# Kernel tuning notes

Hardware: AMD Instinct MI355X
Metric: run time of the kernel (lower is better)

The kernel has to match this reference:

```python
import jax, jax.numpy as jnp
import numpy as np

B, L, DL, DM, K = 8192, 1, 1024, 1024, 8


def setup_inputs() -> dict:
    key = jax.random.key(0)
    ks = jax.random.split(key, 8)
    s = lambda k, shape, sc=1.0: jax.random.normal(k, shape, jnp.float32) * sc
    return {
        "l_hidden": s(ks[0], (B, L, DL)),
        "m_hidden": s(ks[1], (B, L, DM)),
        "G_l_m": s(ks[2], (DL, K, DM)),   # randn'd each fwd in torch; exposed as input
        "G_m_l": s(ks[3], (DM, K, DL)),
        "l_fc1_w": s(ks[4], (256, DL), 0.02),
        "l_fc1_b": jnp.zeros((256,), jnp.float32),
        "l_fc2_w": s(ks[5], (DL, 256), 0.02),
        "l_fc2_b": jnp.zeros((DL,), jnp.float32),
        "m_fc1_w": s(ks[6], (128, DM), 0.02),
        "m_fc1_b": jnp.zeros((128,), jnp.float32),
        "m_fc2_w": s(ks[7], (DM, 128), 0.02),
        "m_fc2_b": jnp.zeros((DM,), jnp.float32),
    }


def _cross(h_a, h_b, G, g_vec):
    """One direction of the cross-share unit.
    h_a: [B,L,Da], h_b: [B,L,Db], G: [Da,K,Db], g_vec: [B,L,Da]. L must be 1.
    Broadcasts G over batch instead of torch's .repeat (same math, no 256GB copy).
    """
    b, l, da = h_a.shape
    k = G.shape[1]
    # l_hidden @ reshape(G, [Da, K*Db]) -> reshape to [B, L*K, Db]
    s = jnp.einsum('bld,dke->blke', h_a, G).reshape(b, l * k, -1)      # [B,L*K,Db]
    # tanh( shared @ h_b^T ) -> [B, L*K, L]
    t = jnp.tanh(jnp.einsum('bke,bse->bks', s, h_b))                    # [B,L*K,L]
    # reshape [B,L,K,L] -> permute [B,L,L,K] -> [B,L*L,K]
    t = t.reshape(b, l, k, l).transpose(0, 1, 3, 2).reshape(b, l * l, k)
    g = jnp.tile(g_vec, (1, k, 1))                                      # [B,L*K,Da] (L=1 -> [B,K,Da])
    vec = jnp.matmul(t, g)                                              # [B,L*L,Da]
    attn = jax.nn.softmax(vec, axis=-1)
    out = h_a + attn * h_a
    return out, attn


def reference(l_hidden, m_hidden, G_l_m, G_m_l,
              l_fc1_w, l_fc1_b, l_fc2_w, l_fc2_b,
              m_fc1_w, m_fc1_b, m_fc2_w, m_fc2_b):
    # dropout(0.3) is identity in eval mode
    G_vec_l = (l_hidden @ l_fc1_w.T + l_fc1_b) @ l_fc2_w.T + l_fc2_b   # [B,L,DL]
    G_vec_m = (m_hidden @ m_fc1_w.T + m_fc1_b) @ m_fc2_w.T + m_fc2_b   # [B,L,DM]
    l_out, l_attn = _cross(l_hidden, m_hidden, G_l_m, G_vec_l)
    m_out, m_attn = _cross(m_hidden, l_hidden, G_m_l, G_vec_m)
    return l_out, m_out, l_attn, m_attn
```

## Files before the change

### kernel.cpp

```cpp
#include <hip/hip_runtime.h>


#define NB 8192
#define DD 1024

typedef __bf16 bf16x8 __attribute__((ext_vector_type(8)));
typedef float f32x4 __attribute__((ext_vector_type(4)));

__device__ __forceinline__ unsigned short f2bf(float f) {
  unsigned u = __float_as_uint(f);
  u += 0x7FFFu + ((u >> 16) & 1u);
  return (unsigned short)(u >> 16);
}
__device__ __forceinline__ float bf2f(unsigned short h) {
  return __uint_as_float(((unsigned)h) << 16);
}

__global__ __launch_bounds__(256) void split_cast_k(
    const float* __restrict__ in, unsigned short* __restrict__ hi,
    unsigned short* __restrict__ lo, int n4) {
  int i = blockIdx.x * 256 + threadIdx.x;
  if (i >= n4) return;
  float4 v = reinterpret_cast<const float4*>(in)[i];
  float vv[4] = {v.x, v.y, v.z, v.w};
  unsigned short hh[4], ll[4];
#pragma unroll
  for (int c = 0; c < 4; ++c) {
    hh[c] = f2bf(vv[c]);
    ll[c] = f2bf(vv[c] - bf2f(hh[c]));
  }
  reinterpret_cast<ushort4*>(hi)[i] = make_ushort4(hh[0], hh[1], hh[2], hh[3]);
  reinterpret_cast<ushort4*>(lo)[i] = make_ushort4(ll[0], ll[1], ll[2], ll[3]);
}

__global__ __launch_bounds__(256) void transpose_split_k(
    const float* __restrict__ G, unsigned short* __restrict__ bhi,
    unsigned short* __restrict__ blo) {
  __shared__ float t[32][33];
  int c0 = blockIdx.x * 32;
  int d0 = blockIdx.y * 32;
  int tx = threadIdx.x & 31;
  int tg = threadIdx.x >> 5;
#pragma unroll
  for (int s = 0; s < 4; ++s) {
    int dr = tg * 4 + s;
    t[dr][tx] = G[(size_t)(d0 + dr) * 8192 + c0 + tx];
  }
  __syncthreads();
#pragma unroll
  for (int s = 0; s < 4; ++s) {
    int cr = tg * 4 + s;
    float v = t[tx][cr];
    size_t o = (size_t)(c0 + cr) * 1024 + d0 + tx;
    unsigned short h = f2bf(v);
    bhi[o] = h;
    blo[o] = f2bf(v - bf2f(h));
  }
}

__global__ __launch_bounds__(256) void wct_k(
    const float* __restrict__ w1, const float* __restrict__ b1,
    const float* __restrict__ w2, const float* __restrict__ b2, int J,
    unsigned short* __restrict__ bhi, unsigned short* __restrict__ blo,
    float* __restrict__ bc) {
  __shared__ float w2row[256];
  int n = blockIdx.x;
  int tid = threadIdx.x;
  if (tid < J) w2row[tid] = w2[n * J + tid];
  __syncthreads();
#pragma unroll
  for (int s = 0; s < 4; ++s) {
    int i = tid + s * 256;
    float acc = 0.f;
    for (int j = 0; j < J; ++j) acc = fmaf(w2row[j], w1[j * 1024 + i], acc);
    size_t o = (size_t)(8192 + n) * 1024 + i;
    unsigned short h = f2bf(acc);
    bhi[o] = h;
    blo[o] = f2bf(acc - bf2f(h));
  }
  if (tid == 0) {
    float acc = 0.f;
    for (int j = 0; j < J; ++j) acc = fmaf(w2row[j], b1[j], acc);
    bc[n] = acc + b2[n];
  }
}

#define SBAR() do { asm volatile("" ::: "memory"); __builtin_amdgcn_s_barrier(); asm volatile("" ::: "memory"); } while (0)
#define WAITV0() asm volatile("s_waitcnt vmcnt(0)" ::: "memory")

#define GLOAD(SRC, DST)                                              \
  __builtin_amdgcn_global_load_lds(                                  \
      (const __attribute__((address_space(1))) void*)(SRC),          \
      (__attribute__((address_space(3))) void*)(lds + (DST)), 16, 0, 0)

__global__ __launch_bounds__(512, 1) void gemm_k(
    const unsigned short* __restrict__ Ahi_, const unsigned short* __restrict__ Alo_,
    const unsigned short* __restrict__ Bhi_, const unsigned short* __restrict__ Blo_,
    const float* __restrict__ hb, float* __restrict__ gvec, float* __restrict__ x) {
  __shared__ __align__(16) char lds[131072];
  const char* Ah = (const char*)Ahi_;
  const char* Al = (const char*)Alo_;
  const char* Bh = (const char*)Bhi_;
  const char* Bl = (const char*)Blo_;

  const int tid = threadIdx.x;
  const int lane = tid & 63;
  const int wid = tid >> 6;
  const int wm = wid >> 2, wn = wid & 3;

  const int bid = blockIdx.x;
  const int xcd = bid & 7;
  const int j = bid >> 3;
  const int by = xcd * 4 + (j & 3);
  const int bx = j >> 2;
  const int m0 = by * 256;
  const int n0 = bx * 256;
  const bool isg = (n0 >= 8192);
  const int nt = isg ? 16 : 48;

  const int rowl = tid >> 3;
  const int colsw = ((tid & 7) ^ ((tid >> 3) & 7)) << 4;
  const int s0 = ((lane >> 4) ^ (lane & 7)) << 4;
  const int s1 = s0 ^ 64;

  f32x4 acc[4][4][2] = {};

  auto stage = [&](int tl, int par, int q) {
    const int seg = tl >> 4;
    const char* mat;
    int rowbase, dst;
    if (q < 2) {
      mat = (seg == 1) ? Al : Ah;
      rowbase = m0 + q * 128;
      dst = par * 32768 + q * 16384;
    } else {
      mat = (seg == 2) ? Bl : Bh;
      rowbase = n0 + (q - 2) * 128;
      dst = 65536 + par * 32768 + (q - 2) * 16384;
    }
    const char* src = mat + (size_t)(rowbase + rowl) * 2048 + ((tl & 15) << 7) + colsw;
    dst += wid * 1024;
    GLOAD(src, dst);
    GLOAD(src + 64 * 2048, dst + 8192);
  };

  auto ldA = [&](bf16x8 (*d)[2], int qa, int cb) {
    const char* p = lds + cb + qa * 16384 + (wm * 64 + (lane & 15)) * 128;
#pragma unroll
    for (int f = 0; f < 4; ++f) {
      d[f][0] = *reinterpret_cast<const bf16x8*>(p + f * 2048 + s0);
      d[f][1] = *reinterpret_cast<const bf16x8*>(p + f * 2048 + s1);
    }
  };
  auto ldB = [&](bf16x8 (*d)[2], int qb, int cb) {
    const char* p = lds + 65536 + cb + qb * 16384 + (wn * 32 + (lane & 15)) * 128;
#pragma unroll
    for (int g = 0; g < 2; ++g) {
      d[g][0] = *reinterpret_cast<const bf16x8*>(p + g * 2048 + s0);
      d[g][1] = *reinterpret_cast<const bf16x8*>(p + g * 2048 + s1);
    }
  };
  auto mm = [&](f32x4 (*ac)[2], bf16x8 (*aa)[2], bf16x8 (*bb)[2]) {
#pragma unroll
    for (int f = 0; f < 4; ++f)
#pragma unroll
      for (int g = 0; g < 2; ++g) {
        ac[f][g] = __builtin_amdgcn_mfma_f32_16x16x32_bf16(aa[f][0], bb[g][0], ac[f][g], 0, 0, 0);
        ac[f][g] = __builtin_amdgcn_mfma_f32_16x16x32_bf16(aa[f][1], bb[g][1], ac[f][g], 0, 0, 0);
      }
  };

  bf16x8 af[4][2], af2[4][2], bv[2][2], bv2[2][2];

  stage(0, 0, 0); stage(0, 0, 2); stage(0, 0, 1); stage(0, 0, 3);
  WAITV0();
  SBAR();
  ldA(af, 0, 0);
  ldB(bv, 0, 0);

  for (int t = 0; t < nt; ++t) {
    const int cb = (t & 1) * 32768;
    const int cbN = cb ^ 32768;
    const int parN = (t + 1) & 1;
    const int tn = (t + 1 < nt) ? (t + 1) : (nt - 1);
    ldB(bv2, 1, cb);
    stage(tn, parN, 0);
    stage(tn, parN, 2);
    __builtin_amdgcn_s_setprio(1);
    mm(acc[0], af, bv);
    __builtin_amdgcn_s_setprio(0);
    ldA(af2, 1, cb);
    __builtin_amdgcn_s_setprio(1);
    mm(acc[1], af, bv2);
    __builtin_amdgcn_s_setprio(0);
    WAITV0();
    SBAR();
    ldA(af, 0, cbN);
    stage(tn, parN, 1);
    stage(tn, parN, 3);
    __builtin_amdgcn_s_setprio(1);
    mm(acc[2], af2, bv2);
    __builtin_amdgcn_s_setprio(0);
    __builtin_amdgcn_s_setprio(1);
    mm(acc[3], af2, bv);
    __builtin_amdgcn_s_setprio(0);
    __builtin_amdgcn_sched_barrier(0);
    ldB(bv, 0, cbN);
    WAITV0();
    SBAR();
  }

  const int coll = lane & 15;
  const int rg = (lane >> 4) * 4;
  if (isg) {
#pragma unroll
    for (int q = 0; q < 4; ++q) {
      const int qm = (q >= 2);
      const int qn = (q == 1 || q == 2);
#pragma unroll
      for (int f = 0; f < 4; ++f)
#pragma unroll
        for (int rr = 0; rr < 4; ++rr) {
          const int row = m0 + qm * 128 + wm * 64 + f * 16 + rg + rr;
#pragma unroll
          for (int g = 0; g < 2; ++g) {
            const int gcol = (n0 - 8192) + qn * 128 + wn * 32 + g * 16 + coll;
            gvec[(size_t)row * 1024 + gcol] = acc[q][f][g][rr];
          }
        }
    }
  } else {
    const int kidx = n0 >> 10;
    const int ebase = (n0 & 1023) + wn * 32 + coll;
#pragma unroll
    for (int qm = 0; qm < 2; ++qm) {
      f32x4 (*acA)[2] = acc[qm ? 3 : 0];
      f32x4 (*acB)[2] = acc[qm ? 2 : 1];
#pragma unroll
      for (int f = 0; f < 4; ++f)
#pragma unroll
        for (int rr = 0; rr < 4; ++rr) {
          const int row = m0 + qm * 128 + wm * 64 + f * 16 + rg + rr;
          const float* hr = hb + (size_t)row * 1024 + ebase;
          float tmp = acA[f][0][rr] * hr[0] + acA[f][1][rr] * hr[16] +
                      acB[f][0][rr] * hr[128] + acB[f][1][rr] * hr[144];
#pragma unroll
          for (int s = 1; s < 16; s <<= 1) tmp += __shfl_xor(tmp, s);
          if (coll == 0) atomicAdd(&x[row * 8 + kidx], tmp);
        }
    }
  }
}

__global__ __launch_bounds__(256) void finalize_k(
    const float* __restrict__ xk, const float* __restrict__ gvec,
    const float* __restrict__ bc, const float* __restrict__ ha,
    float* __restrict__ out, float* __restrict__ attn) {
  int b = blockIdx.x;
  int tid = threadIdx.x;
  float S = 0.f;
#pragma unroll
  for (int k = 0; k < 8; ++k) S += tanhf(xk[b * 8 + k]);
  float v[4];
  float mx = -3.4e38f;
#pragma unroll
  for (int s = 0; s < 4; ++s) {
    int d = tid + s * 256;
    v[s] = S * (gvec[(size_t)b * 1024 + d] + bc[d]);
    mx = fmaxf(mx, v[s]);
  }
  __shared__ float red[8];
#pragma unroll
  for (int off = 32; off >= 1; off >>= 1) mx = fmaxf(mx, __shfl_xor(mx, off));
  int lane = tid & 63, w = tid >> 6;
  if (lane == 0) red[w] = mx;
  __syncthreads();
  float m = fmaxf(fmaxf(red[0], red[1]), fmaxf(red[2], red[3]));
  float e[4], sum = 0.f;
#pragma unroll
  for (int s = 0; s < 4; ++s) { e[s] = __expf(v[s] - m); sum += e[s]; }
#pragma unroll
  for (int off = 32; off >= 1; off >>= 1) sum += __shfl_xor(sum, off);
  if (lane == 0) red[4 + w] = sum;
  __syncthreads();
  float inv = 1.f / (red[4] + red[5] + red[6] + red[7]);
#pragma unroll
  for (int s = 0; s < 4; ++s) {
    int d = tid + s * 256;
    float a = e[s] * inv;
    attn[(size_t)b * 1024 + d] = a;
    float h = ha[(size_t)b * 1024 + d];
    out[(size_t)b * 1024 + d] = fmaf(a, h, h);
  }
}

extern "C" void kernel_launch(void* const* d_in, const int* in_sizes, int n_in,
                              void* d_out, int out_size, void* d_ws, size_t ws_size,
                              hipStream_t stream) {
  const float* l_hidden = (const float*)d_in[0];
  const float* m_hidden = (const float*)d_in[1];
  const float* G_l_m = (const float*)d_in[2];
  const float* G_m_l = (const float*)d_in[3];
  const float* l_fc1_w = (const float*)d_in[4];
  const float* l_fc1_b = (const float*)d_in[5];
  const float* l_fc2_w = (const float*)d_in[6];
  const float* l_fc2_b = (const float*)d_in[7];
  const float* m_fc1_w = (const float*)d_in[8];
  const float* m_fc1_b = (const float*)d_in[9];
  const float* m_fc2_w = (const float*)d_in[10];
  const float* m_fc2_b = (const float*)d_in[11];
  float* out = (float*)d_out;

  char* ws = (char*)d_ws;
  unsigned short* Ahi = (unsigned short*)(ws);
  unsigned short* Alo = (unsigned short*)(ws + 16777216);
  unsigned short* Bhi = (unsigned short*)(ws + 33554432);
  unsigned short* Blo = (unsigned short*)(ws + 52428800);
  float* gvec = (float*)(ws + 71303168);
  float* x = (float*)(ws + 104857600);
  float* bc = (float*)(ws + 105381888);

  hipMemsetAsync(x, 0, 2 * NB * 8 * sizeof(float), stream);

  const size_t BD = (size_t)NB * DD;
  dim3 gemmGrid(1152);

  split_cast_k<<<(int)(BD / 4 / 256), 256, 0, stream>>>(l_hidden, Ahi, Alo, (int)(BD / 4));
  transpose_split_k<<<dim3(256, 32), 256, 0, stream>>>(G_l_m, Bhi, Blo);
  wct_k<<<1024, 256, 0, stream>>>(l_fc1_w, l_fc1_b, l_fc2_w, l_fc2_b, 256, Bhi, Blo, bc);
  gemm_k<<<gemmGrid, 512, 0, stream>>>(Ahi, Alo, Bhi, Blo, m_hidden, gvec, x);
  finalize_k<<<NB, 256, 0, stream>>>(x, gvec, bc, l_hidden, out, out + 2 * BD);

  split_cast_k<<<(int)(BD / 4 / 256), 256, 0, stream>>>(m_hidden, Ahi, Alo, (int)(BD / 4));
  transpose_split_k<<<dim3(256, 32), 256, 0, stream>>>(G_m_l, Bhi, Blo);
  wct_k<<<1024, 256, 0, stream>>>(m_fc1_w, m_fc1_b, m_fc2_w, m_fc2_b, 128, Bhi, Blo, bc);
  gemm_k<<<gemmGrid, 512, 0, stream>>>(Ahi, Alo, Bhi, Blo, l_hidden, gvec, x + NB * 8);
  finalize_k<<<NB, 256, 0, stream>>>(x + NB * 8, gvec, bc, m_hidden, out + BD, out + 3 * BD);
}
```

Baseline: 1.054 ms.

## Pre-swizzle B into MFMA fragment layout and load it directly to registers

The B operand (transposed G plus the folded FC weights) is now written in a fragment-tiled layout, so each wave can read its MFMA B fragments straight from global memory into registers. B no longer passes through LDS, which halves LDS use and removes the B staging and LDS reads. Waits are relaxed to vmcnt(4) so the direct B loads can stay in flight across the barrier. In exchange, each wave issues its own global loads for B with no sharing through LDS, which adds L2 traffic and exposes global latency in the MFMA loop.

Result: slower. 1.173 ms (+11.3%).

```diff
diff --git a/kernel.cpp b/kernel.cpp
--- a/kernel.cpp
+++ b/kernel.cpp
@@ -14,6 +14,11 @@
 }
 __device__ __forceinline__ float bf2f(unsigned short h) {
   return __uint_as_float(((unsigned)h) << 16);
+}
+
+__device__ __forceinline__ size_t bidx(int n, int k) {
+  return ((size_t)(n >> 4) << 14) + ((k >> 5) << 9) + (((k >> 3) & 3) << 7) +
+         ((n & 15) << 3) + (k & 7);
 }
 
 __global__ __launch_bounds__(256) void split_cast_k(
@@ -51,7 +56,7 @@
   for (int s = 0; s < 4; ++s) {
     int cr = tg * 4 + s;
     float v = t[tx][cr];
-    size_t o = (size_t)(c0 + cr) * 1024 + d0 + tx;
+    size_t o = bidx(c0 + cr, d0 + tx);
     unsigned short h = f2bf(v);
     bhi[o] = h;
     blo[o] = f2bf(v - bf2f(h));
@@ -73,7 +78,7 @@
     int i = tid + s * 256;
     float acc = 0.f;
     for (int j = 0; j < J; ++j) acc = fmaf(w2row[j], w1[j * 1024 + i], acc);
-    size_t o = (size_t)(8192 + n) * 1024 + i;
+    size_t o = bidx(8192 + n, i);
     unsigned short h = f2bf(acc);
     bhi[o] = h;
     blo[o] = f2bf(acc - bf2f(h));
@@ -87,6 +92,7 @@
 
 #define SBAR() do { asm volatile("" ::: "memory"); __builtin_amdgcn_s_barrier(); asm volatile("" ::: "memory"); } while (0)
 #define WAITV0() asm volatile("s_waitcnt vmcnt(0)" ::: "memory")
+#define WAITV4() asm volatile("s_waitcnt vmcnt(4)" ::: "memory")
 
 #define GLOAD(SRC, DST)                                              \
   __builtin_amdgcn_global_load_lds(                                  \
@@ -97,7 +103,7 @@
     const unsigned short* __restrict__ Ahi_, const unsigned short* __restrict__ Alo_,
     const unsigned short* __restrict__ Bhi_, const unsigned short* __restrict__ Blo_,
     const float* __restrict__ hb, float* __restrict__ gvec, float* __restrict__ x) {
-  __shared__ __align__(16) char lds[131072];
+  __shared__ __align__(16) char lds[65536];
   const char* Ah = (const char*)Ahi_;
   const char* Al = (const char*)Alo_;
   const char* Bh = (const char*)Bhi_;
@@ -126,20 +132,9 @@
   f32x4 acc[4][4][2] = {};
 
   auto stage = [&](int tl, int par, int q) {
-    const int seg = tl >> 4;
-    const char* mat;
-    int rowbase, dst;
-    if (q < 2) {
-      mat = (seg == 1) ? Al : Ah;
-      rowbase = m0 + q * 128;
-      dst = par * 32768 + q * 16384;
-    } else {
-      mat = (seg == 2) ? Bl : Bh;
-      rowbase = n0 + (q - 2) * 128;
-      dst = 65536 + par * 32768 + (q - 2) * 16384;
-    }
-    const char* src = mat + (size_t)(rowbase + rowl) * 2048 + ((tl & 15) << 7) + colsw;
-    dst += wid * 1024;
+    const char* mat = ((tl >> 4) == 1) ? Al : Ah;
+    const char* src = mat + (size_t)(m0 + q * 128 + rowl) * 2048 + ((tl & 15) << 7) + colsw;
+    const int dst = par * 32768 + q * 16384 + wid * 1024;
     GLOAD(src, dst);
     GLOAD(src + 64 * 2048, dst + 8192);
   };
@@ -152,12 +147,15 @@
       d[f][1] = *reinterpret_cast<const bf16x8*>(p + f * 2048 + s1);
     }
   };
-  auto ldB = [&](bf16x8 (*d)[2], int qb, int cb) {
-    const char* p = lds + 65536 + cb + qb * 16384 + (wn * 32 + (lane & 15)) * 128;
+  auto ldBdir = [&](bf16x8 (*d)[2], int qn, int tl) {
+    const char* base = ((tl >> 4) == 2) ? Bl : Bh;
 #pragma unroll
     for (int g = 0; g < 2; ++g) {
-      d[g][0] = *reinterpret_cast<const bf16x8*>(p + g * 2048 + s0);
-      d[g][1] = *reinterpret_cast<const bf16x8*>(p + g * 2048 + s1);
+      const size_t chunk =
+          ((size_t)(n0 >> 4) + qn * 8 + wn * 2 + g) * 32 + ((tl & 15) << 1);
+      const char* p = base + chunk * 1024 + lane * 16;
+      d[g][0] = *reinterpret_cast<const bf16x8*>(p);
+      d[g][1] = *reinterpret_cast<const bf16x8*>(p + 1024);
     }
   };
   auto mm = [&](f32x4 (*ac)[2], bf16x8 (*aa)[2], bf16x8 (*bb)[2]) {
@@ -172,20 +170,20 @@
 
   bf16x8 af[4][2], af2[4][2], bv[2][2], bv2[2][2];
 
-  stage(0, 0, 0); stage(0, 0, 2); stage(0, 0, 1); stage(0, 0, 3);
-  WAITV0();
+  stage(0, 0, 0); stage(0, 0, 1);
+  ldBdir(bv, 0, 0);
+  __builtin_amdgcn_sched_barrier(0);
+  WAITV4();
   SBAR();
   ldA(af, 0, 0);
-  ldB(bv, 0, 0);
 
   for (int t = 0; t < nt; ++t) {
     const int cb = (t & 1) * 32768;
     const int cbN = cb ^ 32768;
     const int parN = (t + 1) & 1;
     const int tn = (t + 1 < nt) ? (t + 1) : (nt - 1);
-    ldB(bv2, 1, cb);
+    ldBdir(bv2, 1, t);
     stage(tn, parN, 0);
-    stage(tn, parN, 2);
     __builtin_amdgcn_s_setprio(1);
     mm(acc[0], af, bv);
     __builtin_amdgcn_s_setprio(0);
@@ -197,7 +195,6 @@
     SBAR();
     ldA(af, 0, cbN);
     stage(tn, parN, 1);
-    stage(tn, parN, 3);
     __builtin_amdgcn_s_setprio(1);
     mm(acc[2], af2, bv2);
     __builtin_amdgcn_s_setprio(0);
@@ -205,8 +202,9 @@
     mm(acc[3], af2, bv);
     __builtin_amdgcn_s_setprio(0);
     __builtin_amdgcn_sched_barrier(0);
-    ldB(bv, 0, cbN);
-    WAITV0();
+    ldBdir(bv, 0, tn);
+    __builtin_amdgcn_sched_barrier(0);
+    WAITV4();
     SBAR();
   }
 
```
